# Kernel tuning notes

Hardware: AMD Instinct MI355X
Metric: run time of the kernel (lower is better)

Reference implementation:

```python
import jax, jax.numpy as jnp
import numpy as np

B, S, W, V, E, H, T = 512, 512, 3, 100000, 128, 100, 64
PAD = 0


def setup_inputs() -> dict:
    key = jax.random.key(0)
    ks = jax.random.split(key, 10)
    inputs = jax.random.randint(ks[0], (B, S, W), 0, V)          # word feature ids
    tags = jax.random.randint(ks[1], (B, S), 0, T)
    emb_table = jax.random.normal(ks[2], (V, E), jnp.float32) * 0.1
    W1 = jax.random.normal(ks[3], (E, H), jnp.float32) * (1.0 / np.sqrt(E))
    b1 = jnp.zeros((H,), jnp.float32)
    W2 = jax.random.normal(ks[4], (H, T), jnp.float32) * (1.0 / np.sqrt(H))
    b2 = jnp.zeros((T,), jnp.float32)
    start_trans = jax.random.uniform(ks[5], (T,), jnp.float32, -0.1, 0.1)
    end_trans = jax.random.uniform(ks[6], (T,), jnp.float32, -0.1, 0.1)
    transitions = jax.random.uniform(ks[7], (T, T), jnp.float32, -0.1, 0.1)
    return {"inputs": inputs, "tags": tags, "emb_table": emb_table,
            "W1": W1, "b1": b1, "W2": W2, "b2": b2,
            "start_trans": start_trans, "end_trans": end_trans,
            "transitions": transitions}


def reference(inputs, tags, emb_table, W1, b1, W2, b2,
              start_trans, end_trans, transitions):
    # mask: token is real if any word feature != padding_idx. [S,B] (time-major)
    mask = (jnp.sum(inputs != PAD, axis=-1) != 0).T
    # Emission scorer (dropout disabled = eval/deterministic)
    emb = jnp.take(emb_table, inputs, axis=0).sum(axis=2)        # [B,S,E]
    h = jnp.tanh(emb @ W1 + b1)                                  # [B,S,H]
    em = (h @ W2 + b2).transpose(1, 0, 2)                        # [S,B,T]
    tags_t = tags.T                                              # [S,B]
    maskf = mask.astype(em.dtype)
    b_idx = jnp.arange(em.shape[1])

    # ---- numerator: score of the gold tag path ----
    score = start_trans[tags_t[0]] + em[0, b_idx, tags_t[0]]     # [B]
    trans_sc = transitions[tags_t[:-1], tags_t[1:]]              # [S-1,B]
    em_sc = jnp.take_along_axis(em[1:], tags_t[1:, :, None], axis=2)[..., 0]
    score = score + jnp.sum((trans_sc + em_sc) * maskf[1:], axis=0)
    seq_ends = jnp.sum(mask.astype(jnp.int32), axis=0) - 1       # [B]
    last_tags = tags_t[seq_ends, b_idx]
    numerator = score + end_trans[last_tags]

    # ---- denominator: log partition via forward algorithm (log-semiring scan) ----
    alpha0 = start_trans[None, :] + em[0]                        # [B,T]

    def step(alpha, x):
        em_t, m_t = x                                            # [B,T], [B]
        nxt = jax.nn.logsumexp(
            alpha[:, :, None] + transitions[None, :, :] + em_t[:, None, :],
            axis=1)                                              # [B,T]
        return jnp.where(m_t[:, None], nxt, alpha), None

    alpha, _ = jax.lax.scan(step, alpha0, (em[1:], mask[1:]))
    denominator = jax.nn.logsumexp(alpha + end_trans[None, :], axis=1)

    # loss = -log-likelihood, per batch element (reduce=False)
    return denominator - numerator
```

## Files before the change

### kernel.cpp

```cpp
#include <hip/hip_runtime.h>

#define B_ 512
#define S_ 512
#define E_ 128
#define H_ 100
#define T_ 64
#define V_ 100000
#define BS_ (B_*S_)

typedef __attribute__((ext_vector_type(8))) short bf16x8;
typedef __attribute__((ext_vector_type(4))) float f32x4;
typedef _Float16 h2 __attribute__((ext_vector_type(2)));
union U16x4 { uint4 u; bf16x8 s; };

__device__ __forceinline__ unsigned f2bf1(float x){
    unsigned u = __float_as_uint(x);
    return (u + 0x7FFFu + ((u>>16)&1u)) >> 16;
}
__device__ __forceinline__ float bf2f(unsigned short h){
    return __uint_as_float(((unsigned)h)<<16);
}
__device__ __forceinline__ float rfl_f(float x){
    return __uint_as_float(__builtin_amdgcn_readfirstlane(__float_as_uint(x)));
}
__device__ __forceinline__ unsigned addpack3(unsigned a, unsigned b, unsigned c){
    float lo = __uint_as_float(a<<16) + __uint_as_float(b<<16) + __uint_as_float(c<<16);
    float hi = __uint_as_float(a&0xFFFF0000u) + __uint_as_float(b&0xFFFF0000u)
             + __uint_as_float(c&0xFFFF0000u);
    return f2bf1(lo) | (f2bf1(hi)<<16);
}
__device__ __forceinline__ float fdot2h(unsigned u, h2 e, float c){
    h2 p; __builtin_memcpy(&p, &u, 4);
#if __has_builtin(__builtin_amdgcn_fdot2)
    return __builtin_amdgcn_fdot2(p, e, c, false);
#else
    return fmaf((float)p.x, (float)e.x, fmaf((float)p.y, (float)e.y, c));
#endif
}

__global__ __launch_bounds__(256) void prep_tbl(
    const float* __restrict__ tbl, uint2* __restrict__ tblh)
{
    int idx = blockIdx.x*256 + threadIdx.x;
    if (idx < (V_*E_)/4) {
        float4 v = ((const float4*)tbl)[idx];
        uint2 o;
        o.x = f2bf1(v.x) | (f2bf1(v.y)<<16);
        o.y = f2bf1(v.z) | (f2bf1(v.w)<<16);
        tblh[idx] = o;
    }
}

__global__ __launch_bounds__(64) void prep_w(
    const float* __restrict__ W1, const float* __restrict__ W2,
    uint4* __restrict__ W1f, uint4* __restrict__ W2f)
{
    const int idx = blockIdx.x*64 + threadIdx.x;
    if (idx < 7*4*64) {
        int lane = idx & 63, kt = (idx>>6)&3, nt = idx>>8;
        int n = nt*16 + (lane&15);
        int kb = kt*32 + (lane>>4)*8;
        unsigned wv[4];
        #pragma unroll
        for (int p = 0; p < 4; ++p) {
            float v0 = (n < H_) ? W1[(kb+2*p  )*H_ + n] : 0.f;
            float v1 = (n < H_) ? W1[(kb+2*p+1)*H_ + n] : 0.f;
            wv[p] = f2bf1(v0) | (f2bf1(v1) << 16);
        }
        W1f[idx] = make_uint4(wv[0],wv[1],wv[2],wv[3]);
    } else {
        int id2 = idx - 7*4*64;
        int lane = id2 & 63, kt = (id2>>6)&3, nt = id2>>8;
        int n = nt*16 + (lane&15);
        int kb = kt*32 + (lane>>4)*8;
        unsigned wv[4];
        #pragma unroll
        for (int p = 0; p < 4; ++p) {
            int k0 = kb+2*p, k1 = kb+2*p+1;
            float v0 = (k0 < H_) ? W2[k0*T_ + n] : 0.f;
            float v1 = (k1 < H_) ? W2[k1*T_ + n] : 0.f;
            wv[p] = f2bf1(v0) | (f2bf1(v1) << 16);
        }
        W2f[id2] = make_uint4(wv[0],wv[1],wv[2],wv[3]);
    }
}

__global__ __launch_bounds__(128)
__attribute__((amdgpu_waves_per_eu(1, 1)))
void fused_kernel(
    const int* __restrict__ inputs, const int* __restrict__ tags,
    const unsigned short* __restrict__ tblh,
    const float* __restrict__ b1, const float* __restrict__ b2,
    const uint4* __restrict__ W1f, const uint4* __restrict__ W2f,
    const float* __restrict__ start_trans, const float* __restrict__ end_trans,
    const float* __restrict__ trans, float* __restrict__ out)
{
    __shared__ uint4 sW1f[1792];
    __shared__ uint4 sW2f[1024];
    __shared__ __align__(16) unsigned short ring[2][4][512];
    __shared__ uint4 sA2[2][256];
    __shared__ __align__(16) _Float16 pbufH[2][T_];
    __shared__ float pubB[T_];
    __shared__ float fnum[2];
    __shared__ int   icnt[2];
    __shared__ float lsB_sh;

    const int b   = blockIdx.x;
    const int tid = threadIdx.x;
    const int w   = tid >> 6;
    const int j   = tid & 63;
    const int col = j & 15;
    const int hi  = j >> 4;
    const int rowin = hi * 4;
    const int* tags_b = tags + b*S_;
    const int* in_b   = inputs + (size_t)b*S_*3;

    for (int i = tid; i < 1792; i += 128) sW1f[i] = W1f[i];
    for (int i = tid; i < 1024; i += 128) sW2f[i] = W2f[i];

    unsigned long long mball[4];
    #pragma unroll
    for (int g4 = 0; g4 < 4; ++g4) {
        int t = (w*4 + g4)*64 + j;
        int a0 = in_b[t*3+0], a1 = in_b[t*3+1], a2 = in_b[t*3+2];
        mball[g4] = __ballot((a0 | a1 | a2) != 0);
    }
    int cnt = 0;
    #pragma unroll
    for (int g4 = 0; g4 < 4; ++g4) cnt += __popcll(mball[g4]);
    if (j == 0) icnt[w] = cnt;
    if (w == 0) mball[0] &= ~1ull;

    __syncthreads();

    float bv1[7], bv2[4];
    #pragma unroll
    for (int nt = 0; nt < 7; ++nt) { int n = nt*16+col; bv1[nt] = (n < H_) ? b1[n] : 0.f; }
    #pragma unroll
    for (int nt2 = 0; nt2 < 4; ++nt2) bv2[nt2] = b2[nt2*16+col];

    h2 E2[32];
    #pragma unroll
    for (int i = 0; i < 32; ++i) {
        h2 e;
        if (w == 0) { e.x = (_Float16)__expf(trans[(2*i)*T_ + j]);
                      e.y = (_Float16)__expf(trans[(2*i+1)*T_ + j]); }
        else        { e.x = (_Float16)__expf(trans[j*T_ + 2*i]);
                      e.y = (_Float16)__expf(trans[j*T_ + 2*i+1]); }
        E2[i] = e;
    }

    auto baseOf = [&](int p){ return w ? (480 - 16*p) : 16*p; };

    float np = 0.f;

    auto loadIdx = [&](int p, int& x, int& y, int& z){
        size_t rgg = (size_t)b*S_ + (size_t)(baseOf(p) + col);
        x = in_b[(rgg - (size_t)b*S_)*3 + 0];
        y = in_b[(rgg - (size_t)b*S_)*3 + 1];
        z = in_b[(rgg - (size_t)b*S_)*3 + 2];
    };
    auto issueGathers = [&](int i0, int i1, int i2, uint4* g){
        const unsigned short* tr0 = tblh + (size_t)i0*E_;
        const unsigned short* tr1 = tblh + (size_t)i1*E_;
        const unsigned short* tr2 = tblh + (size_t)i2*E_;
        #pragma unroll
        for (int kt = 0; kt < 4; ++kt) {
            int off = kt*32 + hi*8;
            g[kt*3+0] = *(const uint4*)(tr0 + off);
            g[kt*3+1] = *(const uint4*)(tr1 + off);
            g[kt*3+2] = *(const uint4*)(tr2 + off);
        }
    };

    auto produce = [&](int p, const uint4* g){
        U16x4 a[4];
        #pragma unroll
        for (int kt = 0; kt < 4; ++kt)
            a[kt].u = make_uint4(
                addpack3(g[kt*3+0].x, g[kt*3+1].x, g[kt*3+2].x),
                addpack3(g[kt*3+0].y, g[kt*3+1].y, g[kt*3+2].y),
                addpack3(g[kt*3+0].z, g[kt*3+1].z, g[kt*3+2].z),
                addpack3(g[kt*3+0].w, g[kt*3+1].w, g[kt*3+2].w));

        f32x4 acc1[7];
        #pragma unroll
        for (int nt = 0; nt < 7; ++nt) {
            f32x4 c; c[0]=bv1[nt]; c[1]=bv1[nt]; c[2]=bv1[nt]; c[3]=bv1[nt];
            #pragma unroll
            for (int k = 0; k < 4; ++k) {
                U16x4 bfr; bfr.u = sW1f[(nt*4+k)*64 + j];
                c = __builtin_amdgcn_mfma_f32_16x16x32_bf16(a[k].s, bfr.s, c, 0,0,0);
            }
            acc1[nt] = c;
        }
        #pragma unroll
        for (int nt = 0; nt < 7; ++nt)
            #pragma unroll
            for (int rr = 0; rr < 4; ++rr) {
                float x = acc1[nt][rr];
                acc1[nt][rr] = 1.f - 2.f/(__expf(2.f*x)+1.f);
            }

        if (j >= 32) sA2[w][3*64 + j] = make_uint4(0,0,0,0);
        unsigned short* A2h = (unsigned short*)sA2[w];
        #pragma unroll
        for (int nt = 0; nt < 7; ++nt)
            #pragma unroll
            for (int rr = 0; rr < 4; ++rr) {
                int k2 = nt*16 + col;
                int kt2 = k2 >> 5, g2 = (k2>>3)&3, i2v = k2&7;
                int u4idx = kt2*64 + g2*16 + (rowin + rr);
                A2h[u4idx*8 + i2v] = (unsigned short)f2bf1(acc1[nt][rr]);
            }
        __builtin_amdgcn_wave_barrier();

        U16x4 a2[4];
        #pragma unroll
        for (int k = 0; k < 4; ++k) a2[k].u = sA2[w][k*64 + j];
        __builtin_amdgcn_wave_barrier();

        unsigned short* tbuf = (unsigned short*)sA2[w];
        #pragma unroll
        for (int nt2 = 0; nt2 < 4; ++nt2) {
            f32x4 c; c[0]=bv2[nt2]; c[1]=bv2[nt2]; c[2]=bv2[nt2]; c[3]=bv2[nt2];
            #pragma unroll
            for (int k = 0; k < 4; ++k) {
                U16x4 bfr; bfr.u = sW2f[(nt2*4+k)*64 + j];
                c = __builtin_amdgcn_mfma_f32_16x16x32_bf16(a2[k].s, bfr.s, c, 0,0,0);
            }
            #pragma unroll
            for (int rr = 0; rr < 4; ++rr)
                tbuf[(rowin+rr)*72 + nt2*16 + col] = (unsigned short)f2bf1(c[rr]);
        }
        __builtin_amdgcn_wave_barrier();

        {
            const int rl = j >> 2;
            const int ch = (j & 3) * 2;
            const uint4* t4 = (const uint4*)tbuf;
            uint4 u0 = t4[rl*9 + ch];
            uint4 u1 = t4[rl*9 + ch + 1];
            int row = baseOf(p) + rl;
            int grp = row >> 3;
            int kidx = w ? (63 - grp) : grp;
            uint4* dst = (uint4*)&ring[w][kidx & 3][(row & 7)*64];
            dst[ch]   = u0;
            dst[ch+1] = u1;
        }
        __builtin_amdgcn_wave_barrier();

        if (j < 16) {
            int t = baseOf(p) + j;
            if (t >= 1) {
                int word = (t >> 6) - w*4;
                if ((mball[word] >> (t & 63)) & 1ull) {
                    int tp = tags_b[t-1], tc = tags_b[t];
                    int grp = t >> 3;
                    int kidx = w ? (63 - grp) : grp;
                    np += trans[tp*T_ + tc] + bf2f(ring[w][kidx & 3][(t & 7)*64 + tc]);
                }
            }
        }
    };

    uint4 g[12];
    int i0, i1, i2, ni0, ni1, ni2;
    loadIdx(0, i0, i1, i2);
    issueGathers(i0, i1, i2, g);
    produce(0, g);
    float a, ls;
    if (w == 0) {
        if (j == 0) {
            int tag0 = tags_b[0];
            np += start_trans[tag0] + bf2f(ring[0][0][tag0]);
        }
        float x0v = start_trans[j] + bf2f(ring[0][0][j]);
        ls = rfl_f(x0v);
        a  = __expf(x0v - ls);
    } else {
        a  = __expf(end_trans[j]);
        ls = 0.f;
    }
    loadIdx(1, i0, i1, i2);
    issueGathers(i0, i1, i2, g);
    produce(1, g);
    loadIdx(2, i0, i1, i2);
    issueGathers(i0, i1, i2, g);
    loadIdx(3, ni0, ni1, ni2);

    float eg[8];
    #pragma unroll
    for (int s = 0; s < 8; ++s)
        eg[s] = __expf(bf2f(ring[w][0][(w ? (7-s) : s)*64 + j]));

    for (int p = 0; p < 16; ++p) {
        #pragma unroll
        for (int kk = 0; kk < 2; ++kk) {
            const int k = 2*p + kk;
            unsigned short raw16[8];
            if (k < 31) {
                const unsigned short* nxt = ring[w][(k+1) & 3];
                #pragma unroll
                for (int s = 0; s < 8; ++s)
                    raw16[s] = nxt[(w ? (7-s) : s)*64 + j];
            }
            const int ag = w ? (63 - k) : k;
            const unsigned mg = (unsigned)((mball[(ag>>3) - w*4] >> ((ag&7)*8)) & 0xFFull);

            #pragma unroll
            for (int s = 0; s < 8; ++s) {
                float wv = (w == 0) ? a : (eg[s] * a);
                pbufH[w][j] = (_Float16)(wv * 0.015625f);
                __builtin_amdgcn_wave_barrier();
                float sc   = rfl_f(a);
                float sinv = __builtin_amdgcn_rcpf(sc);
                float logs = __logf(sc);
                float keep = a * sinv;
                float dmul = ((w == 0) ? (eg[s] * sinv) : sinv) * 64.0f;

                const uint4* ph = (const uint4*)pbufH[w];
                float ac0=0.f, ac1=0.f, ac2=0.f, ac3=0.f;
                #pragma unroll
                for (int q = 0; q < 8; ++q) {
                    uint4 U = ph[q];
                    ac0 = fdot2h(U.x, E2[4*q+0], ac0);
                    ac1 = fdot2h(U.y, E2[4*q+1], ac1);
                    ac2 = fdot2h(U.z, E2[4*q+2], ac2);
                    ac3 = fdot2h(U.w, E2[4*q+3], ac3);
                }
                float dot = (ac0+ac1)+(ac2+ac3);
                float cand = dot * dmul;
                const int bit = (w == 0) ? s : (7 - s);
                a = ((mg >> bit) & 1u) ? cand : keep;
                ls += logs;
                __builtin_amdgcn_wave_barrier();
            }
            if (k < 31) {
                #pragma unroll
                for (int s = 0; s < 8; ++s) eg[s] = __expf(bf2f(raw16[s]));
            }
        }
        if (p <= 13) produce(p + 2, g);
        if (p <= 12) {
            issueGathers(ni0, ni1, ni2, g);
            if (p <= 11) loadIdx(p + 4, ni0, ni1, ni2);
        }
    }

    #pragma unroll
    for (int off = 32; off >= 1; off >>= 1) np += __shfl_xor(np, off, 64);
    if (j == 0) fnum[w] = np;

    if (w == 1) {
        pubB[j] = a;
        if (j == 0) lsB_sh = ls;
    }
    __syncthreads();
    if (w == 0) {
        float x = a * pubB[j];
        #pragma unroll
        for (int off = 32; off >= 1; off >>= 1) x += __shfl_xor(x, off, 64);
        int mcount = icnt[0] + icnt[1];
        int se = mcount - 1; if (se < 0) se = 0;
        const int last_tag = tags_b[se];
        float numer = fnum[0] + fnum[1] + end_trans[last_tag];
        if (j == 0) out[b] = ls + lsB_sh + __logf(x) - numer;
    }
}

extern "C" void kernel_launch(void* const* d_in, const int* in_sizes, int n_in,
                              void* d_out, int out_size, void* d_ws, size_t ws_size,
                              hipStream_t stream) {
    const int*   inputs      = (const int*)  d_in[0];
    const int*   tags        = (const int*)  d_in[1];
    const float* emb_table   = (const float*)d_in[2];
    const float* W1          = (const float*)d_in[3];
    const float* b1          = (const float*)d_in[4];
    const float* W2          = (const float*)d_in[5];
    const float* b2          = (const float*)d_in[6];
    const float* start_trans = (const float*)d_in[7];
    const float* end_trans   = (const float*)d_in[8];
    const float* transitions = (const float*)d_in[9];
    float* out = (float*)d_out;

    unsigned short* tblh = (unsigned short*)d_ws;
    uint4* W1f = (uint4*)((char*)d_ws + (size_t)V_*E_*2);
    uint4* W2f = W1f + 7*4*64;

    prep_tbl<<<dim3((V_*E_/4 + 255)/256), dim3(256), 0, stream>>>(emb_table, (uint2*)tblh);
    prep_w<<<dim3((7*4*64 + 4*4*64)/64), dim3(64), 0, stream>>>(W1, W2, W1f, W2f);
    fused_kernel<<<dim3(B_), dim3(128), 0, stream>>>(
        inputs, tags, tblh, b1, b2, W1f, W2f,
        start_trans, end_trans, transitions, out);
}
```

Baseline: 239.6 us.

## Split per-lane 64-term forward dot product across lane quads with DPP reduction

Each lane previously computed its full 64-element transition dot product serially, reading all 8 uint4 of the shared probability buffer. Now every lane in a quad handles a 16-element slice for four output tags, so it reads only 2 uint4. The four partial sums are then combined with DPP xor-1/xor-2 swaps in a transpose-reduce. The E2 exp(transitions) register layout is reshuffled to match. This aims to shorten the serial latency chain and cut LDS reads in the recurrence step, at the cost of cross-lane DPP operations and selects.

After: 222.4 us. 7.2% less time.

```diff
diff --git a/kernel.cpp b/kernel.cpp
--- a/kernel.cpp
+++ b/kernel.cpp
@@ -36,6 +36,12 @@
 #else
     return fmaf((float)p.x, (float)e.x, fmaf((float)p.y, (float)e.y, c));
 #endif
+}
+__device__ __forceinline__ float dpp_xor1(float x){
+    return __int_as_float(__builtin_amdgcn_mov_dpp(__float_as_int(x), 0xB1, 0xF, 0xF, true));
+}
+__device__ __forceinline__ float dpp_xor2(float x){
+    return __int_as_float(__builtin_amdgcn_mov_dpp(__float_as_int(x), 0x4E, 0xF, 0xF, true));
 }
 
 __global__ __launch_bounds__(256) void prep_tbl(
@@ -112,6 +118,10 @@
     const int col = j & 15;
     const int hi  = j >> 4;
     const int rowin = hi * 4;
+    const int qg  = j >> 2;
+    const int qm  = j & 3;
+    const bool qb0 = (j & 1) != 0;
+    const bool qb1 = (j & 2) != 0;
     const int* tags_b = tags + b*S_;
     const int* in_b   = inputs + (size_t)b*S_*3;
 
@@ -141,24 +151,23 @@
 
     h2 E2[32];
     #pragma unroll
-    for (int i = 0; i < 32; ++i) {
-        h2 e;
-        if (w == 0) { e.x = (_Float16)__expf(trans[(2*i)*T_ + j]);
-                      e.y = (_Float16)__expf(trans[(2*i+1)*T_ + j]); }
-        else        { e.x = (_Float16)__expf(trans[j*T_ + 2*i]);
-                      e.y = (_Float16)__expf(trans[j*T_ + 2*i+1]); }
-        E2[i] = e;
-    }
+    for (int o = 0; o < 4; ++o)
+        #pragma unroll
+        for (int i = 0; i < 8; ++i) {
+            int r0, c0, r1, c1;
+            if (w == 0) { r0 = 16*qm + 2*i; c0 = 4*qg + o; r1 = r0 + 1; c1 = c0; }
+            else        { r0 = 4*qg + o; c0 = 16*qm + 2*i; r1 = r0; c1 = c0 + 1; }
+            h2 e; e.x = (_Float16)__expf(trans[r0*T_ + c0]);
+                  e.y = (_Float16)__expf(trans[r1*T_ + c1]);
+            E2[o*8 + i] = e;
+        }
 
     auto baseOf = [&](int p){ return w ? (480 - 16*p) : 16*p; };
-
     float np = 0.f;
 
     auto loadIdx = [&](int p, int& x, int& y, int& z){
-        size_t rgg = (size_t)b*S_ + (size_t)(baseOf(p) + col);
-        x = in_b[(rgg - (size_t)b*S_)*3 + 0];
-        y = in_b[(rgg - (size_t)b*S_)*3 + 1];
-        z = in_b[(rgg - (size_t)b*S_)*3 + 2];
+        int t = baseOf(p) + col;
+        x = in_b[t*3 + 0]; y = in_b[t*3 + 1]; z = in_b[t*3 + 2];
     };
     auto issueGathers = [&](int i0, int i1, int i2, uint4* g){
         const unsigned short* tr0 = tblh + (size_t)i0*E_;
@@ -320,17 +329,37 @@
                 float dmul = ((w == 0) ? (eg[s] * sinv) : sinv) * 64.0f;
 
                 const uint4* ph = (const uint4*)pbufH[w];
-                float ac0=0.f, ac1=0.f, ac2=0.f, ac3=0.f;
-                #pragma unroll
-                for (int q = 0; q < 8; ++q) {
-                    uint4 U = ph[q];
-                    ac0 = fdot2h(U.x, E2[4*q+0], ac0);
-                    ac1 = fdot2h(U.y, E2[4*q+1], ac1);
-                    ac2 = fdot2h(U.z, E2[4*q+2], ac2);
-                    ac3 = fdot2h(U.w, E2[4*q+3], ac3);
-                }
-                float dot = (ac0+ac1)+(ac2+ac3);
-                float cand = dot * dmul;
+                uint4 U0 = ph[2*qm];
+                uint4 U1 = ph[2*qm + 1];
+                float p0, p1, p2, p3;
+                p0 = fdot2h(U0.x, E2[ 0], 0.f);  p0 = fdot2h(U0.y, E2[ 1], p0);
+                p0 = fdot2h(U0.z, E2[ 2], p0);   p0 = fdot2h(U0.w, E2[ 3], p0);
+                p0 = fdot2h(U1.x, E2[ 4], p0);   p0 = fdot2h(U1.y, E2[ 5], p0);
+                p0 = fdot2h(U1.z, E2[ 6], p0);   p0 = fdot2h(U1.w, E2[ 7], p0);
+                p1 = fdot2h(U0.x, E2[ 8], 0.f);  p1 = fdot2h(U0.y, E2[ 9], p1);
+                p1 = fdot2h(U0.z, E2[10], p1);   p1 = fdot2h(U0.w, E2[11], p1);
+                p1 = fdot2h(U1.x, E2[12], p1);   p1 = fdot2h(U1.y, E2[13], p1);
+                p1 = fdot2h(U1.z, E2[14], p1);   p1 = fdot2h(U1.w, E2[15], p1);
+                p2 = fdot2h(U0.x, E2[16], 0.f);  p2 = fdot2h(U0.y, E2[17], p2);
+                p2 = fdot2h(U0.z, E2[18], p2);   p2 = fdot2h(U0.w, E2[19], p2);
+                p2 = fdot2h(U1.x, E2[20], p2);   p2 = fdot2h(U1.y, E2[21], p2);
+                p2 = fdot2h(U1.z, E2[22], p2);   p2 = fdot2h(U1.w, E2[23], p2);
+                p3 = fdot2h(U0.x, E2[24], 0.f);  p3 = fdot2h(U0.y, E2[25], p3);
+                p3 = fdot2h(U0.z, E2[26], p3);   p3 = fdot2h(U0.w, E2[27], p3);
+                p3 = fdot2h(U1.x, E2[28], p3);   p3 = fdot2h(U1.y, E2[29], p3);
+                p3 = fdot2h(U1.z, E2[30], p3);   p3 = fdot2h(U1.w, E2[31], p3);
+
+                float t0 = qb1 ? p2 : p0;
+                float t1 = qb1 ? p3 : p1;
+                float s0 = qb1 ? p0 : p2;
+                float s1 = qb1 ? p1 : p3;
+                t0 += dpp_xor2(s0);
+                t1 += dpp_xor2(s1);
+                float tt = qb0 ? t1 : t0;
+                float ss = qb0 ? t0 : t1;
+                float y  = tt + dpp_xor1(ss);
+
+                float cand = y * dmul;
                 const int bit = (w == 0) ? s : (7 - s);
                 a = ((mg >> bit) & 1u) ? cand : keep;
                 ls += logs;
```

## Split forward-scan dot product across lanes with DPP butterfly reduction

Applied to the files above, without the earlier changes.

Each lane of the log-semiring recurrence now reads one 16-byte chunk of the scaled alpha vector from LDS instead of all eight. It computes partial dot products for eight output tags against a transposed exp(transitions) register layout. The partials are then combined with a three-stage xor-butterfly of DPP moves and selects. This is meant to cut LDS traffic and latency on the serial per-timestep critical path, at the cost of extra cross-lane moves and selects. The token-base offset for the reverse-direction wave also changes, and the index-loading lambda is simplified.

Result: faster. 228.0 us (-4.8%).

```diff
diff --git a/kernel.cpp b/kernel.cpp
--- a/kernel.cpp
+++ b/kernel.cpp
@@ -36,6 +36,15 @@
 #else
     return fmaf((float)p.x, (float)e.x, fmaf((float)p.y, (float)e.y, c));
 #endif
+}
+__device__ __forceinline__ float dpp_xor1(float x){
+    return __int_as_float(__builtin_amdgcn_mov_dpp(__float_as_int(x), 0xB1, 0xF, 0xF, true));
+}
+__device__ __forceinline__ float dpp_xor2(float x){
+    return __int_as_float(__builtin_amdgcn_mov_dpp(__float_as_int(x), 0x4E, 0xF, 0xF, true));
+}
+__device__ __forceinline__ float dpp_xor7(float x){
+    return __int_as_float(__builtin_amdgcn_mov_dpp(__float_as_int(x), 0x141, 0xF, 0xF, true));
 }
 
 __global__ __launch_bounds__(256) void prep_tbl(
@@ -112,6 +121,11 @@
     const int col = j & 15;
     const int hi  = j >> 4;
     const int rowin = hi * 4;
+    const int qm8 = j & 7;
+    const int qg8 = j >> 3;
+    const bool qb0 = (j & 1) != 0;
+    const bool qb1 = (j & 2) != 0;
+    const bool qb2 = (j & 4) != 0;
     const int* tags_b = tags + b*S_;
     const int* in_b   = inputs + (size_t)b*S_*3;
 
@@ -141,24 +155,23 @@
 
     h2 E2[32];
     #pragma unroll
-    for (int i = 0; i < 32; ++i) {
-        h2 e;
-        if (w == 0) { e.x = (_Float16)__expf(trans[(2*i)*T_ + j]);
-                      e.y = (_Float16)__expf(trans[(2*i+1)*T_ + j]); }
-        else        { e.x = (_Float16)__expf(trans[j*T_ + 2*i]);
-                      e.y = (_Float16)__expf(trans[j*T_ + 2*i+1]); }
-        E2[i] = e;
-    }
-
-    auto baseOf = [&](int p){ return w ? (480 - 16*p) : 16*p; };
-
+    for (int o = 0; o < 8; ++o)
+        #pragma unroll
+        for (int i2 = 0; i2 < 4; ++i2) {
+            int r0, c0, r1, c1;
+            if (w == 0) { r0 = 8*qm8 + 2*i2; c0 = 8*qg8 + o; r1 = r0 + 1; c1 = c0; }
+            else        { r0 = 8*qg8 + o; c0 = 8*qm8 + 2*i2; r1 = r0; c1 = c0 + 1; }
+            h2 e; e.x = (_Float16)__expf(trans[r0*T_ + c0]);
+                  e.y = (_Float16)__expf(trans[r1*T_ + c1]);
+            E2[o*4 + i2] = e;
+        }
+
+    auto baseOf = [&](int p){ return w ? (496 - 16*p) : 16*p; };
     float np = 0.f;
 
     auto loadIdx = [&](int p, int& x, int& y, int& z){
-        size_t rgg = (size_t)b*S_ + (size_t)(baseOf(p) + col);
-        x = in_b[(rgg - (size_t)b*S_)*3 + 0];
-        y = in_b[(rgg - (size_t)b*S_)*3 + 1];
-        z = in_b[(rgg - (size_t)b*S_)*3 + 2];
+        int t = baseOf(p) + col;
+        x = in_b[t*3 + 0]; y = in_b[t*3 + 1]; z = in_b[t*3 + 2];
     };
     auto issueGathers = [&](int i0, int i1, int i2, uint4* g){
         const unsigned short* tr0 = tblh + (size_t)i0*E_;
@@ -320,17 +333,32 @@
                 float dmul = ((w == 0) ? (eg[s] * sinv) : sinv) * 64.0f;
 
                 const uint4* ph = (const uint4*)pbufH[w];
-                float ac0=0.f, ac1=0.f, ac2=0.f, ac3=0.f;
+                uint4 U = ph[qm8];
+                float pp[8];
                 #pragma unroll
-                for (int q = 0; q < 8; ++q) {
-                    uint4 U = ph[q];
-                    ac0 = fdot2h(U.x, E2[4*q+0], ac0);
-                    ac1 = fdot2h(U.y, E2[4*q+1], ac1);
-                    ac2 = fdot2h(U.z, E2[4*q+2], ac2);
-                    ac3 = fdot2h(U.w, E2[4*q+3], ac3);
+                for (int o = 0; o < 8; ++o) {
+                    float acc = fdot2h(U.x, E2[o*4+0], 0.f);
+                    acc = fdot2h(U.y, E2[o*4+1], acc);
+                    acc = fdot2h(U.z, E2[o*4+2], acc);
+                    acc = fdot2h(U.w, E2[o*4+3], acc);
+                    pp[o] = acc;
                 }
-                float dot = (ac0+ac1)+(ac2+ac3);
-                float cand = dot * dmul;
+                float k0 = qb2 ? pp[4] : pp[0], s0 = qb2 ? pp[0] : pp[4];
+                float k1 = qb2 ? pp[5] : pp[1], s1 = qb2 ? pp[1] : pp[5];
+                float k2v = qb2 ? pp[6] : pp[2], s2 = qb2 ? pp[2] : pp[6];
+                float k3 = qb2 ? pp[7] : pp[3], s3 = qb2 ? pp[3] : pp[7];
+                k0 += dpp_xor7(s0);
+                k1 += dpp_xor7(s1);
+                k2v += dpp_xor7(s2);
+                k3 += dpp_xor7(s3);
+                float m0 = qb1 ? k2v : k0, n0 = qb1 ? k0 : k2v;
+                float m1 = qb1 ? k3 : k1, n1 = qb1 ? k1 : k3;
+                m0 += dpp_xor2(n0);
+                m1 += dpp_xor2(n1);
+                float uu = qb0 ? m1 : m0, vv = qb0 ? m0 : m1;
+                float y  = uu + dpp_xor1(vv);
+
+                float cand = y * dmul;
                 const int bit = (w == 0) ? s : (7 - s);
                 a = ((mg >> bit) & 1u) ? cand : keep;
                 ls += logs;
```
